# Performance work log

Measured on AMD Instinct MI355X. Metric: run time of the kernel, lower is better.

The kernel has to match this reference:

```python
import jax, jax.numpy as jnp
import numpy as np

B, L, D = 1, 4096, 1024
H = 16
HD = D // H
SCALE = HD ** -0.5


def setup_inputs() -> dict:
    key = jax.random.key(0)
    k1, k2, k3 = jax.random.split(key, 3)
    X = jax.random.normal(k1, (B, L, D), dtype=jnp.float32)
    # torch Linear default init ~ U(-1/sqrt(fan_in), 1/sqrt(fan_in)); scaled normals are fine for a reference
    Wqkv = jax.random.normal(k2, (D, 3 * D), dtype=jnp.float32) * (D ** -0.5)
    bqkv = jnp.zeros((3 * D,), dtype=jnp.float32)
    Wproj = jax.random.normal(k3, (D, D), dtype=jnp.float32) * (D ** -0.5)
    bproj = jnp.zeros((D,), dtype=jnp.float32)
    return {"X": X, "Wqkv": Wqkv, "bqkv": bqkv, "Wproj": Wproj, "bproj": bproj}


def reference(X, Wqkv, bqkv, Wproj, bproj):
    Bn, Ln, Dn = X.shape
    qkv = X @ Wqkv + bqkv                       # [B, L, 3D]
    qkv = qkv.reshape(Bn, Ln, 3, H, HD)
    q, k, v = qkv[:, :, 0], qkv[:, :, 1], qkv[:, :, 2]   # [B, L, H, HD]
    # attention scores [B, H, L, L] (naive, matches original)
    attn = jnp.einsum('bqhd,bkhd->bhqk', q, k) * SCALE
    causal = jnp.tril(jnp.ones((Ln, Ln), dtype=bool))     # True = keep
    attn = jnp.where(causal, attn, -jnp.inf)
    score = jax.nn.softmax(attn, axis=-1)
    out = jnp.einsum('bhqk,bkhd->bqhd', score, v)         # [B, L, H, HD]
    out = out.reshape(Bn, Ln, Dn)
    return out @ Wproj + bproj
```

## Files before the change

kernel.cpp:

```cpp
#include <hip/hip_runtime.h>
#include <hip/hip_bf16.h>


typedef unsigned short ushort_t;
typedef __attribute__((ext_vector_type(8))) short short8;
typedef __attribute__((ext_vector_type(4))) float f32x4;

#define MFMA16(a, b, c) __builtin_amdgcn_mfma_f32_16x16x32_bf16(a, b, c, 0, 0, 0)

static constexpr int Lq = 4096;
static constexpr int Dm = 1024;
static constexpr int NH = 16;
static constexpr int HD = 64;
static constexpr int D3 = 3072;
static constexpr float SCALE_LOG2E = 0.125f * 1.44269504088896340736f;

__device__ __forceinline__ ushort_t f2bf(float f) {
    union { float f; unsigned int u; } x{f};
    unsigned int u = x.u;
    u += 0x7fffu + ((u >> 16) & 1u);
    return (ushort_t)(u >> 16);
}

__device__ __forceinline__ void gl2lds16(const ushort_t* g, ushort_t* l) {
    __builtin_amdgcn_global_load_lds(
        (const __attribute__((address_space(1))) unsigned int*)g,
        (__attribute__((address_space(3))) unsigned int*)l, 16, 0, 0);
}

__global__ void cvt_bf16(const float* __restrict__ in, ushort_t* __restrict__ out, int n) {
    int i = (blockIdx.x * blockDim.x + threadIdx.x) * 4;
    if (i + 3 < n) {
        float4 v = *(const float4*)&in[i];
        ushort_t r[4] = { f2bf(v.x), f2bf(v.y), f2bf(v.z), f2bf(v.w) };
        *(uint2*)&out[i] = *(uint2*)r;
    }
}

__global__ void wtrans(const float* __restrict__ W, ushort_t* __restrict__ Wt, int K, int N) {
    __shared__ float tile[32][33];
    int nb = blockIdx.x * 32, kb = blockIdx.y * 32;
    int tx = threadIdx.x, ty = threadIdx.y;
    for (int j = 0; j < 32; j += 8)
        tile[ty + j][tx] = W[(size_t)(kb + ty + j) * N + nb + tx];
    __syncthreads();
    for (int j = 0; j < 32; j += 8)
        Wt[(size_t)(nb + ty + j) * K + kb + tx] = f2bf(tile[tx][ty + j]);
}

__global__ void vtrans(const ushort_t* __restrict__ qkv, ushort_t* __restrict__ Vt) {
    __shared__ ushort_t tile[32][33];
    int h  = blockIdx.z;
    int lb = blockIdx.x * 32;
    int db = blockIdx.y * 32;
    int tx = threadIdx.x, ty = threadIdx.y;
    for (int j = 0; j < 32; j += 8)
        tile[ty + j][tx] = qkv[(size_t)(lb + ty + j) * D3 + 2048 + h * HD + db + tx];
    __syncthreads();
    for (int j = 0; j < 32; j += 8)
        Vt[(size_t)h * HD * Lq + (size_t)(db + ty + j) * Lq + lb + tx] = tile[tx][ty + j];
}

template <bool OUT_BF16, bool QSCALE>
__global__ void __launch_bounds__(256)
gemm_bt(const ushort_t* __restrict__ A, const ushort_t* __restrict__ Bt,
        const float* __restrict__ bias, void* __restrict__ C,
        int M, int N, int K) {
    __shared__ alignas(16) ushort_t Alds[128 * 32];
    __shared__ alignas(16) ushort_t Blds[128 * 32];
    const int tid  = threadIdx.x;
    const int lane = tid & 63;
    const int w    = tid >> 6;
    const int quad = lane >> 4;
    const int l16  = lane & 15;
    const int mbase = blockIdx.x * 128;
    const int nbase = blockIdx.y * 128;
    const int moff  = (w >> 1) * 64;
    const int noff  = (w & 1) * 64;

    f32x4 acc[4][4] = {};

    for (int kb = 0; kb < K; kb += 32) {
        __syncthreads();
        #pragma unroll
        for (int c = 0; c < 2; c++) {
            int id  = w * 128 + c * 64 + lane;
            int row = id >> 2, col = (id & 3) * 8;
            gl2lds16(&A[(size_t)(mbase + row) * K + kb + col], &Alds[(size_t)(w * 128 + c * 64) * 8]);
            gl2lds16(&Bt[(size_t)(nbase + row) * K + kb + col], &Blds[(size_t)(w * 128 + c * 64) * 8]);
        }
        __syncthreads();
        short8 a[4], b[4];
        #pragma unroll
        for (int m = 0; m < 4; m++)
            a[m] = *(const short8*)&Alds[(moff + m * 16 + l16) * 32 + quad * 8];
        #pragma unroll
        for (int n = 0; n < 4; n++)
            b[n] = *(const short8*)&Blds[(noff + n * 16 + l16) * 32 + quad * 8];
        #pragma unroll
        for (int m = 0; m < 4; m++)
            #pragma unroll
            for (int n = 0; n < 4; n++)
                acc[m][n] = MFMA16(a[m], b[n], acc[m][n]);
    }

    #pragma unroll
    for (int m = 0; m < 4; m++)
        #pragma unroll
        for (int n = 0; n < 4; n++)
            #pragma unroll
            for (int r = 0; r < 4; r++) {
                int row = mbase + moff + m * 16 + quad * 4 + r;
                int col = nbase + noff + n * 16 + l16;
                float v = acc[m][n][r] + bias[col];
                if (QSCALE && col < Dm) v *= SCALE_LOG2E;
                if (OUT_BF16)
                    ((ushort_t*)C)[(size_t)row * N + col] = f2bf(v);
                else
                    ((float*)C)[(size_t)row * N + col] = v;
            }
}

__global__ void __launch_bounds__(256, 1)
attn_fwd(const ushort_t* __restrict__ qkv, const ushort_t* __restrict__ Vt,
         ushort_t* __restrict__ O) {
    __shared__ alignas(16) ushort_t Kl[2][64 * 64];
    __shared__ alignas(16) ushort_t Vl[2][64 * 64];
    __shared__ alignas(16) ushort_t Pl[4 * 32 * 72];

    const int tid  = threadIdx.x;
    const int lane = tid & 63;
    const int w    = tid >> 6;
    const int quad = lane >> 4;
    const int l16  = lane & 15;
    const int bid  = blockIdx.x;
    const int h    = bid & 15;
    const int p    = bid >> 4;
    ushort_t* pw   = Pl + w * 32 * 72;
    const float NEG_INF = -__builtin_inff();
    const int sw = l16 & 7;

    const short bf1 = (short)0x3F80;
    const short8 ones = { bf1, bf1, bf1, bf1, bf1, bf1, bf1, bf1 };

    const ushort_t* kbase = qkv + Dm + h * HD;
    const ushort_t* vbase = Vt + (size_t)h * HD * Lq;

    const int g0 = w * 128 + lane;
    const int r0 = g0 >> 3, c0 = (g0 & 7) ^ (r0 & 7);
    const int g1 = g0 + 64;
    const int r1 = g1 >> 3, c1 = (g1 & 7) ^ (r1 & 7);
    const ushort_t* ks0 = kbase + (size_t)r0 * D3 + c0 * 8;
    const ushort_t* ks1 = kbase + (size_t)r1 * D3 + c1 * 8;
    const ushort_t* vs0 = vbase + (size_t)r0 * Lq + c0 * 8;
    const ushort_t* vs1 = vbase + (size_t)r1 * Lq + c1 * 8;
    ushort_t* kd0[2] = { &Kl[0][w * 1024], &Kl[1][w * 1024] };
    ushort_t* kd1[2] = { &Kl[0][w * 1024 + 512], &Kl[1][w * 1024 + 512] };
    ushort_t* vd0[2] = { &Vl[0][w * 1024], &Vl[1][w * 1024] };
    ushort_t* vd1[2] = { &Vl[0][w * 1024 + 512], &Vl[1][w * 1024 + 512] };

    for (int sel = 0; sel < 2; sel++) {
        const int c  = sel ? (31 - p) : p;
        const int qc = c * 128;
        const int nt = 2 * c + 2;
        const int qw = qc + w * 32;

        short8 qf[2][2];
        #pragma unroll
        for (int m = 0; m < 2; m++) {
            const ushort_t* qr = qkv + (size_t)(qw + m * 16 + l16) * D3 + h * HD;
            qf[m][0] = *(const short8*)(qr + quad * 8);
            qf[m][1] = *(const short8*)(qr + 32 + quad * 8);
        }

        f32x4 o[2][4] = {};
        f32x4 lacc[2] = {};

        gl2lds16(ks0, kd0[0]);
        gl2lds16(ks1, kd1[0]);
        gl2lds16(vs0, vd0[0]);
        gl2lds16(vs1, vd1[0]);

        for (int kt = 0; kt < nt; kt++) {
            const int buf = kt & 1;
            __syncthreads();
            if (kt + 1 < nt) {
                const size_t ko = (size_t)(kt + 1) * 64 * D3;
                const int    vo = (kt + 1) * 64;
                gl2lds16(ks0 + ko, kd0[buf ^ 1]);
                gl2lds16(ks1 + ko, kd1[buf ^ 1]);
                gl2lds16(vs0 + vo, vd0[buf ^ 1]);
                gl2lds16(vs1 + vo, vd1[buf ^ 1]);
            }
            const int k0 = kt * 64;

            short8 kf[4][2];
            #pragma unroll
            for (int s = 0; s < 4; s++)
                #pragma unroll
                for (int kh = 0; kh < 2; kh++)
                    kf[s][kh] = *(const short8*)&Kl[buf][(s * 16 + l16) * 64 + (((kh * 4 + quad) ^ sw) * 8)];

            f32x4 st[2][4];
            #pragma unroll
            for (int m = 0; m < 2; m++)
                #pragma unroll
                for (int s = 0; s < 4; s++) {
                    f32x4 t = {};
                    t = MFMA16(qf[m][0], kf[s][0], t);
                    t = MFMA16(qf[m][1], kf[s][1], t);
                    st[m][s] = t;
                }

            #pragma unroll
            for (int m = 0; m < 2; m++)
                #pragma unroll
                for (int r = 0; r < 4; r++) {
                    const int qg = qw + m * 16 + quad * 4 + r;
                    ushort_t* prow = pw + (m * 16 + quad * 4 + r) * 72;
                    #pragma unroll
                    for (int s = 0; s < 4; s++) {
                        const int ki = k0 + s * 16 + l16;
                        float v = (ki > qg) ? NEG_INF : st[m][s][r];
                        prow[s * 16 + l16] = f2bf(__builtin_amdgcn_exp2f(v));
                    }
                }

            short8 pf[2][2];
            #pragma unroll
            for (int m = 0; m < 2; m++)
                #pragma unroll
                for (int kh = 0; kh < 2; kh++)
                    pf[m][kh] = *(const short8*)&pw[(m * 16 + l16) * 72 + kh * 32 + quad * 8];
            #pragma unroll
            for (int m = 0; m < 2; m++) {
                lacc[m] = MFMA16(pf[m][0], ones, lacc[m]);
                lacc[m] = MFMA16(pf[m][1], ones, lacc[m]);
            }

            short8 vf[4][2];
            #pragma unroll
            for (int t = 0; t < 4; t++)
                #pragma unroll
                for (int kh = 0; kh < 2; kh++)
                    vf[t][kh] = *(const short8*)&Vl[buf][(t * 16 + l16) * 64 + (((kh * 4 + quad) ^ sw) * 8)];
            #pragma unroll
            for (int m = 0; m < 2; m++)
                #pragma unroll
                for (int t = 0; t < 4; t++) {
                    o[m][t] = MFMA16(pf[m][0], vf[t][0], o[m][t]);
                    o[m][t] = MFMA16(pf[m][1], vf[t][1], o[m][t]);
                }
        }

        #pragma unroll
        for (int m = 0; m < 2; m++)
            #pragma unroll
            for (int r = 0; r < 4; r++) {
                const float inv = 1.0f / lacc[m][r];
                ushort_t* orow = O + (size_t)(qw + m * 16 + quad * 4 + r) * Dm + h * HD;
                #pragma unroll
                for (int t = 0; t < 4; t++)
                    orow[t * 16 + l16] = f2bf(o[m][t][r] * inv);
            }
        __syncthreads();
    }
}

extern "C" void kernel_launch(void* const* d_in, const int* in_sizes, int n_in,
                              void* d_out, int out_size, void* d_ws, size_t ws_size,
                              hipStream_t stream) {
    const float* X     = (const float*)d_in[0];
    const float* Wqkv  = (const float*)d_in[1];
    const float* bqkv  = (const float*)d_in[2];
    const float* Wproj = (const float*)d_in[3];
    const float* bproj = (const float*)d_in[4];
    float* out = (float*)d_out;

    ushort_t* ws     = (ushort_t*)d_ws;
    ushort_t* Xb     = ws;
    ushort_t* WqkvT  = Xb + (size_t)Lq * Dm;
    ushort_t* WprojT = WqkvT + (size_t)D3 * Dm;
    ushort_t* qkvB   = WprojT + (size_t)Dm * Dm;
    ushort_t* VtB    = qkvB + (size_t)Lq * D3;
    ushort_t* Ob     = VtB + (size_t)NH * HD * Lq;

    cvt_bf16<<<(Lq * Dm / 4 + 255) / 256, 256, 0, stream>>>(X, Xb, Lq * Dm);
    wtrans<<<dim3(D3 / 32, Dm / 32), dim3(32, 8), 0, stream>>>(Wqkv, WqkvT, Dm, D3);
    wtrans<<<dim3(Dm / 32, Dm / 32), dim3(32, 8), 0, stream>>>(Wproj, WprojT, Dm, Dm);

    gemm_bt<true, true><<<dim3(Lq / 128, D3 / 128), 256, 0, stream>>>(
        Xb, WqkvT, bqkv, (void*)qkvB, Lq, D3, Dm);

    vtrans<<<dim3(Lq / 32, HD / 32, NH), dim3(32, 8), 0, stream>>>(qkvB, VtB);

    attn_fwd<<<dim3(256), 256, 0, stream>>>(qkvB, VtB, Ob);

    gemm_bt<false, false><<<dim3(Lq / 128, Dm / 128), 256, 0, stream>>>(
        Ob, WprojT, bproj, (void*)out, Lq, Dm, Dm);
}
```

Measured before the change: 237.7 us.

## Use 8 waves per attention block and permute V keys for packed P stores

The attention kernel now runs 512 threads, eight waves of 16 query rows each, instead of four waves of 32 rows. Each thread issues one K and one V async load per tile instead of two of each. The V transpose permutes key order within each 64-key tile so every lane writes four exponentials as a single packed 8-byte LDS store rather than four scalar stores. This adds latency hiding and cuts LDS store instructions, but each wave now reads the full K/V tiles for half as many rows, which doubles LDS read traffic per unit of work.

```diff
diff --git a/kernel.cpp b/kernel.cpp
--- a/kernel.cpp
+++ b/kernel.cpp
@@ -20,6 +20,13 @@
     unsigned int u = x.u;
     u += 0x7fffu + ((u >> 16) & 1u);
     return (ushort_t)(u >> 16);
+}
+
+__device__ __forceinline__ unsigned int pack2bf(float a, float b) {
+    union { float f; unsigned int u; } xa{a}, xb{b};
+    unsigned int ua = xa.u + (0x7fffu + ((xa.u >> 16) & 1u));
+    unsigned int ub = xb.u + (0x7fffu + ((xb.u >> 16) & 1u));
+    return (ua >> 16) | (ub & 0xffff0000u);
 }
 
 __device__ __forceinline__ void gl2lds16(const ushort_t* g, ushort_t* l) {
@@ -57,8 +64,11 @@
     for (int j = 0; j < 32; j += 8)
         tile[ty + j][tx] = qkv[(size_t)(lb + ty + j) * D3 + 2048 + h * HD + db + tx];
     __syncthreads();
-    for (int j = 0; j < 32; j += 8)
-        Vt[(size_t)h * HD * Lq + (size_t)(db + ty + j) * Lq + lb + tx] = tile[tx][ty + j];
+    const int key  = lb + tx;
+    const int k63  = key & 63;
+    const int cp   = (key & ~63) + ((k63 & 15) * 4 + (k63 >> 4));
+    for (int j = 0; j < 32; j += 8)
+        Vt[(size_t)h * HD * Lq + (size_t)(db + ty + j) * Lq + cp] = tile[tx][ty + j];
 }
 
 template <bool OUT_BF16, bool QSCALE>
@@ -121,12 +131,12 @@
             }
 }
 
-__global__ void __launch_bounds__(256, 1)
+__global__ void __launch_bounds__(512, 1)
 attn_fwd(const ushort_t* __restrict__ qkv, const ushort_t* __restrict__ Vt,
          ushort_t* __restrict__ O) {
     __shared__ alignas(16) ushort_t Kl[2][64 * 64];
     __shared__ alignas(16) ushort_t Vl[2][64 * 64];
-    __shared__ alignas(16) ushort_t Pl[4 * 32 * 72];
+    __shared__ alignas(16) ushort_t Pl[8 * 16 * 72];
 
     const int tid  = threadIdx.x;
     const int lane = tid & 63;
@@ -136,7 +146,7 @@
     const int bid  = blockIdx.x;
     const int h    = bid & 15;
     const int p    = bid >> 4;
-    ushort_t* pw   = Pl + w * 32 * 72;
+    ushort_t* pw   = Pl + w * 16 * 72;
     const float NEG_INF = -__builtin_inff();
     const int sw = l16 & 7;
 
@@ -146,51 +156,35 @@
     const ushort_t* kbase = qkv + Dm + h * HD;
     const ushort_t* vbase = Vt + (size_t)h * HD * Lq;
 
-    const int g0 = w * 128 + lane;
-    const int r0 = g0 >> 3, c0 = (g0 & 7) ^ (r0 & 7);
-    const int g1 = g0 + 64;
-    const int r1 = g1 >> 3, c1 = (g1 & 7) ^ (r1 & 7);
-    const ushort_t* ks0 = kbase + (size_t)r0 * D3 + c0 * 8;
-    const ushort_t* ks1 = kbase + (size_t)r1 * D3 + c1 * 8;
-    const ushort_t* vs0 = vbase + (size_t)r0 * Lq + c0 * 8;
-    const ushort_t* vs1 = vbase + (size_t)r1 * Lq + c1 * 8;
-    ushort_t* kd0[2] = { &Kl[0][w * 1024], &Kl[1][w * 1024] };
-    ushort_t* kd1[2] = { &Kl[0][w * 1024 + 512], &Kl[1][w * 1024 + 512] };
-    ushort_t* vd0[2] = { &Vl[0][w * 1024], &Vl[1][w * 1024] };
-    ushort_t* vd1[2] = { &Vl[0][w * 1024 + 512], &Vl[1][w * 1024 + 512] };
+    const int gr = tid;
+    const int rr = gr >> 3, cc = (gr & 7) ^ (rr & 7);
+    const ushort_t* ks = kbase + (size_t)rr * D3 + cc * 8;
+    const ushort_t* vs = vbase + (size_t)rr * Lq + cc * 8;
+    ushort_t* kd[2] = { &Kl[0][w * 512], &Kl[1][w * 512] };
+    ushort_t* vd[2] = { &Vl[0][w * 512], &Vl[1][w * 512] };
 
     for (int sel = 0; sel < 2; sel++) {
         const int c  = sel ? (31 - p) : p;
         const int qc = c * 128;
         const int nt = 2 * c + 2;
-        const int qw = qc + w * 32;
-
-        short8 qf[2][2];
-        #pragma unroll
-        for (int m = 0; m < 2; m++) {
-            const ushort_t* qr = qkv + (size_t)(qw + m * 16 + l16) * D3 + h * HD;
-            qf[m][0] = *(const short8*)(qr + quad * 8);
-            qf[m][1] = *(const short8*)(qr + 32 + quad * 8);
-        }
-
-        f32x4 o[2][4] = {};
-        f32x4 lacc[2] = {};
-
-        gl2lds16(ks0, kd0[0]);
-        gl2lds16(ks1, kd1[0]);
-        gl2lds16(vs0, vd0[0]);
-        gl2lds16(vs1, vd1[0]);
+        const int qw = qc + w * 16;
+
+        const ushort_t* qr = qkv + (size_t)(qw + l16) * D3 + h * HD;
+        const short8 qf0 = *(const short8*)(qr + quad * 8);
+        const short8 qf1 = *(const short8*)(qr + 32 + quad * 8);
+
+        f32x4 o[4] = {};
+        f32x4 lacc = {};
+
+        gl2lds16(ks, kd[0]);
+        gl2lds16(vs, vd[0]);
 
         for (int kt = 0; kt < nt; kt++) {
             const int buf = kt & 1;
             __syncthreads();
             if (kt + 1 < nt) {
-                const size_t ko = (size_t)(kt + 1) * 64 * D3;
-                const int    vo = (kt + 1) * 64;
-                gl2lds16(ks0 + ko, kd0[buf ^ 1]);
-                gl2lds16(ks1 + ko, kd1[buf ^ 1]);
-                gl2lds16(vs0 + vo, vd0[buf ^ 1]);
-                gl2lds16(vs1 + vo, vd1[buf ^ 1]);
+                gl2lds16(ks + (size_t)(kt + 1) * 64 * D3, kd[buf ^ 1]);
+                gl2lds16(vs + (kt + 1) * 64, vd[buf ^ 1]);
             }
             const int k0 = kt * 64;
 
@@ -201,68 +195,50 @@
                 for (int kh = 0; kh < 2; kh++)
                     kf[s][kh] = *(const short8*)&Kl[buf][(s * 16 + l16) * 64 + (((kh * 4 + quad) ^ sw) * 8)];
 
-            f32x4 st[2][4];
-            #pragma unroll
-            for (int m = 0; m < 2; m++)
+            f32x4 st[4];
+            #pragma unroll
+            for (int s = 0; s < 4; s++) {
+                f32x4 t = {};
+                t = MFMA16(qf0, kf[s][0], t);
+                t = MFMA16(qf1, kf[s][1], t);
+                st[s] = t;
+            }
+
+            #pragma unroll
+            for (int r = 0; r < 4; r++) {
+                const int qg = qw + quad * 4 + r;
+                float e[4];
                 #pragma unroll
                 for (int s = 0; s < 4; s++) {
-                    f32x4 t = {};
-                    t = MFMA16(qf[m][0], kf[s][0], t);
-                    t = MFMA16(qf[m][1], kf[s][1], t);
-                    st[m][s] = t;
+                    const int ki = k0 + s * 16 + l16;
+                    e[s] = __builtin_amdgcn_exp2f((ki > qg) ? NEG_INF : st[s][r]);
                 }
-
-            #pragma unroll
-            for (int m = 0; m < 2; m++)
-                #pragma unroll
-                for (int r = 0; r < 4; r++) {
-                    const int qg = qw + m * 16 + quad * 4 + r;
-                    ushort_t* prow = pw + (m * 16 + quad * 4 + r) * 72;
-                    #pragma unroll
-                    for (int s = 0; s < 4; s++) {
-                        const int ki = k0 + s * 16 + l16;
-                        float v = (ki > qg) ? NEG_INF : st[m][s][r];
-                        prow[s * 16 + l16] = f2bf(__builtin_amdgcn_exp2f(v));
-                    }
-                }
-
-            short8 pf[2][2];
-            #pragma unroll
-            for (int m = 0; m < 2; m++)
-                #pragma unroll
-                for (int kh = 0; kh < 2; kh++)
-                    pf[m][kh] = *(const short8*)&pw[(m * 16 + l16) * 72 + kh * 32 + quad * 8];
-            #pragma unroll
-            for (int m = 0; m < 2; m++) {
-                lacc[m] = MFMA16(pf[m][0], ones, lacc[m]);
-                lacc[m] = MFMA16(pf[m][1], ones, lacc[m]);
-            }
-
-            short8 vf[4][2];
+                uint2 pk = { pack2bf(e[0], e[1]), pack2bf(e[2], e[3]) };
+                *(uint2*)&pw[(quad * 4 + r) * 72 + l16 * 4] = pk;
+            }
+
+            const short8 pf0 = *(const short8*)&pw[l16 * 72 + quad * 8];
+            const short8 pf1 = *(const short8*)&pw[l16 * 72 + 32 + quad * 8];
+            lacc = MFMA16(pf0, ones, lacc);
+            lacc = MFMA16(pf1, ones, lacc);
+
+            #pragma unroll
+            for (int t = 0; t < 4; t++) {
+                short8 vf0 = *(const short8*)&Vl[buf][(t * 16 + l16) * 64 + ((quad ^ sw) * 8)];
+                short8 vf1 = *(const short8*)&Vl[buf][(t * 16 + l16) * 64 + (((4 + quad) ^ sw) * 8)];
+                o[t] = MFMA16(pf0, vf0, o[t]);
+                o[t] = MFMA16(pf1, vf1, o[t]);
+            }
+        }
+
+        #pragma unroll
+        for (int r = 0; r < 4; r++) {
+            const float inv = 1.0f / lacc[r];
+            ushort_t* orow = O + (size_t)(qw + quad * 4 + r) * Dm + h * HD;
             #pragma unroll
             for (int t = 0; t < 4; t++)
-                #pragma unroll
-                for (int kh = 0; kh < 2; kh++)
-                    vf[t][kh] = *(const short8*)&Vl[buf][(t * 16 + l16) * 64 + (((kh * 4 + quad) ^ sw) * 8)];
-            #pragma unroll
-            for (int m = 0; m < 2; m++)
-                #pragma unroll
-                for (int t = 0; t < 4; t++) {
-                    o[m][t] = MFMA16(pf[m][0], vf[t][0], o[m][t]);
-                    o[m][t] = MFMA16(pf[m][1], vf[t][1], o[m][t]);
-                }
+                orow[t * 16 + l16] = f2bf(o[t][r] * inv);
         }
-
-        #pragma unroll
-        for (int m = 0; m < 2; m++)
-            #pragma unroll
-            for (int r = 0; r < 4; r++) {
-                const float inv = 1.0f / lacc[m][r];
-                ushort_t* orow = O + (size_t)(qw + m * 16 + quad * 4 + r) * Dm + h * HD;
-                #pragma unroll
-                for (int t = 0; t < 4; t++)
-                    orow[t * 16 + l16] = f2bf(o[m][t][r] * inv);
-            }
         __syncthreads();
     }
 }
@@ -294,7 +270,7 @@
 
     vtrans<<<dim3(Lq / 32, HD / 32, NH), dim3(32, 8), 0, stream>>>(qkvB, VtB);
 
-    attn_fwd<<<dim3(256), 256, 0, stream>>>(qkvB, VtB, Ob);
+    attn_fwd<<<dim3(256), 512, 0, stream>>>(qkvB, VtB, Ob);
 
     gemm_bt<false, false><<<dim3(Lq / 128, Dm / 128), 256, 0, stream>>>(
         Ob, WprojT, bproj, (void*)out, Lq, Dm, Dm);
```

Result: faster. 224.3 us (-5.6%).

## Split attention into one q-chunk per block, peel masked tiles, pack P stores

Applied to the files above, without the earlier changes.

The attention kernel now launches one block per (head, 128-row query chunk), 512 blocks with a two-block occupancy hint, instead of pairing chunks p and 31-p inside one block. Blocks are ordered so the longest chunks start first. The key loop is unrolled by two with static double-buffer indices, and only the final two diagonal tiles apply the causal mask. V^T columns are permuted within each 64-key group so each lane writes its four P values as one packed bf16x2 store, using the hardware convert instead of a manual rounding routine. This trades the built-in load balancing of chunk pairing for more resident blocks and less per-element mask and store work.

```diff
diff --git a/kernel.cpp b/kernel.cpp
--- a/kernel.cpp
+++ b/kernel.cpp
@@ -1,5 +1,6 @@
 #include <hip/hip_runtime.h>
 #include <hip/hip_bf16.h>
+#include <string.h>
 
 
 typedef unsigned short ushort_t;
@@ -20,6 +21,13 @@
     unsigned int u = x.u;
     u += 0x7fffu + ((u >> 16) & 1u);
     return (ushort_t)(u >> 16);
+}
+
+__device__ __forceinline__ unsigned int cvtpk(float a, float b) {
+    __hip_bfloat162 h = __float22bfloat162_rn(make_float2(a, b));
+    unsigned int u;
+    memcpy(&u, &h, 4);
+    return u;
 }
 
 __device__ __forceinline__ void gl2lds16(const ushort_t* g, ushort_t* l) {
@@ -57,8 +65,11 @@
     for (int j = 0; j < 32; j += 8)
         tile[ty + j][tx] = qkv[(size_t)(lb + ty + j) * D3 + 2048 + h * HD + db + tx];
     __syncthreads();
+    const int key  = lb + tx;
+    const int k63  = key & 63;
+    const int cp   = (key & ~63) + ((k63 & 15) * 4 + (k63 >> 4));
     for (int j = 0; j < 32; j += 8)
-        Vt[(size_t)h * HD * Lq + (size_t)(db + ty + j) * Lq + lb + tx] = tile[tx][ty + j];
+        Vt[(size_t)h * HD * Lq + (size_t)(db + ty + j) * Lq + cp] = tile[tx][ty + j];
 }
 
 template <bool OUT_BF16, bool QSCALE>
@@ -121,7 +132,7 @@
             }
 }
 
-__global__ void __launch_bounds__(256, 1)
+__global__ void __launch_bounds__(256, 2)
 attn_fwd(const ushort_t* __restrict__ qkv, const ushort_t* __restrict__ Vt,
          ushort_t* __restrict__ O) {
     __shared__ alignas(16) ushort_t Kl[2][64 * 64];
@@ -135,16 +146,36 @@
     const int l16  = lane & 15;
     const int bid  = blockIdx.x;
     const int h    = bid & 15;
-    const int p    = bid >> 4;
+    const int c    = 31 - (bid >> 4);
+    const int qc   = c * 128;
+    const int qw   = qc + w * 32;
     ushort_t* pw   = Pl + w * 32 * 72;
     const float NEG_INF = -__builtin_inff();
-    const int sw = l16 & 7;
+    const int sw   = l16 & 7;
 
     const short bf1 = (short)0x3F80;
     const short8 ones = { bf1, bf1, bf1, bf1, bf1, bf1, bf1, bf1 };
 
     const ushort_t* kbase = qkv + Dm + h * HD;
     const ushort_t* vbase = Vt + (size_t)h * HD * Lq;
+
+    short8 qf[2][2];
+    #pragma unroll
+    for (int m = 0; m < 2; m++) {
+        const ushort_t* qr = qkv + (size_t)(qw + m * 16 + l16) * D3 + h * HD;
+        qf[m][0] = *(const short8*)(qr + quad * 8);
+        qf[m][1] = *(const short8*)(qr + 32 + quad * 8);
+    }
+
+    f32x4 o[2][4] = {};
+    f32x4 lacc[2] = {};
+
+    int kvo[4][2];
+    #pragma unroll
+    for (int s = 0; s < 4; s++)
+        #pragma unroll
+        for (int kh = 0; kh < 2; kh++)
+            kvo[s][kh] = (s * 16 + l16) * 64 + (((kh * 4 + quad) ^ sw) * 8);
 
     const int g0 = w * 128 + lane;
     const int r0 = g0 >> 3, c0 = (g0 & 7) ^ (r0 & 7);
@@ -154,117 +185,106 @@
     const ushort_t* ks1 = kbase + (size_t)r1 * D3 + c1 * 8;
     const ushort_t* vs0 = vbase + (size_t)r0 * Lq + c0 * 8;
     const ushort_t* vs1 = vbase + (size_t)r1 * Lq + c1 * 8;
-    ushort_t* kd0[2] = { &Kl[0][w * 1024], &Kl[1][w * 1024] };
-    ushort_t* kd1[2] = { &Kl[0][w * 1024 + 512], &Kl[1][w * 1024 + 512] };
-    ushort_t* vd0[2] = { &Vl[0][w * 1024], &Vl[1][w * 1024] };
-    ushort_t* vd1[2] = { &Vl[0][w * 1024 + 512], &Vl[1][w * 1024 + 512] };
-
-    for (int sel = 0; sel < 2; sel++) {
-        const int c  = sel ? (31 - p) : p;
-        const int qc = c * 128;
-        const int nt = 2 * c + 2;
-        const int qw = qc + w * 32;
-
-        short8 qf[2][2];
-        #pragma unroll
-        for (int m = 0; m < 2; m++) {
-            const ushort_t* qr = qkv + (size_t)(qw + m * 16 + l16) * D3 + h * HD;
-            qf[m][0] = *(const short8*)(qr + quad * 8);
-            qf[m][1] = *(const short8*)(qr + 32 + quad * 8);
-        }
-
-        f32x4 o[2][4] = {};
-        f32x4 lacc[2] = {};
-
-        gl2lds16(ks0, kd0[0]);
-        gl2lds16(ks1, kd1[0]);
-        gl2lds16(vs0, vd0[0]);
-        gl2lds16(vs1, vd1[0]);
-
-        for (int kt = 0; kt < nt; kt++) {
-            const int buf = kt & 1;
-            __syncthreads();
-            if (kt + 1 < nt) {
-                const size_t ko = (size_t)(kt + 1) * 64 * D3;
-                const int    vo = (kt + 1) * 64;
-                gl2lds16(ks0 + ko, kd0[buf ^ 1]);
-                gl2lds16(ks1 + ko, kd1[buf ^ 1]);
-                gl2lds16(vs0 + vo, vd0[buf ^ 1]);
-                gl2lds16(vs1 + vo, vd1[buf ^ 1]);
+
+    auto stage = [&](int t, int b) {
+        const size_t ko = (size_t)t * 64 * D3;
+        const int    vo = t * 64;
+        gl2lds16(ks0 + ko, &Kl[b][w * 1024]);
+        gl2lds16(ks1 + ko, &Kl[b][w * 1024 + 512]);
+        gl2lds16(vs0 + vo, &Vl[b][w * 1024]);
+        gl2lds16(vs1 + vo, &Vl[b][w * 1024 + 512]);
+    };
+
+    auto compute = [&](const ushort_t* Kb, const ushort_t* Vb, int k0, bool domask) {
+        short8 kf[4][2];
+        #pragma unroll
+        for (int s = 0; s < 4; s++)
+            #pragma unroll
+            for (int kh = 0; kh < 2; kh++)
+                kf[s][kh] = *(const short8*)&Kb[kvo[s][kh]];
+
+        f32x4 st[2][4];
+        #pragma unroll
+        for (int m = 0; m < 2; m++)
+            #pragma unroll
+            for (int s = 0; s < 4; s++) {
+                f32x4 t = {};
+                t = MFMA16(qf[m][0], kf[s][0], t);
+                t = MFMA16(qf[m][1], kf[s][1], t);
+                st[m][s] = t;
             }
-            const int k0 = kt * 64;
-
-            short8 kf[4][2];
-            #pragma unroll
-            for (int s = 0; s < 4; s++)
-                #pragma unroll
-                for (int kh = 0; kh < 2; kh++)
-                    kf[s][kh] = *(const short8*)&Kl[buf][(s * 16 + l16) * 64 + (((kh * 4 + quad) ^ sw) * 8)];
-
-            f32x4 st[2][4];
-            #pragma unroll
-            for (int m = 0; m < 2; m++)
+
+        #pragma unroll
+        for (int m = 0; m < 2; m++)
+            #pragma unroll
+            for (int r = 0; r < 4; r++) {
+                float e[4];
                 #pragma unroll
                 for (int s = 0; s < 4; s++) {
-                    f32x4 t = {};
-                    t = MFMA16(qf[m][0], kf[s][0], t);
-                    t = MFMA16(qf[m][1], kf[s][1], t);
-                    st[m][s] = t;
+                    float v = st[m][s][r];
+                    if (domask) {
+                        const int qg = qw + m * 16 + quad * 4 + r;
+                        if (k0 + s * 16 + l16 > qg) v = NEG_INF;
+                    }
+                    e[s] = __builtin_amdgcn_exp2f(v);
                 }
-
-            #pragma unroll
-            for (int m = 0; m < 2; m++)
-                #pragma unroll
-                for (int r = 0; r < 4; r++) {
-                    const int qg = qw + m * 16 + quad * 4 + r;
-                    ushort_t* prow = pw + (m * 16 + quad * 4 + r) * 72;
-                    #pragma unroll
-                    for (int s = 0; s < 4; s++) {
-                        const int ki = k0 + s * 16 + l16;
-                        float v = (ki > qg) ? NEG_INF : st[m][s][r];
-                        prow[s * 16 + l16] = f2bf(__builtin_amdgcn_exp2f(v));
-                    }
-                }
-
-            short8 pf[2][2];
-            #pragma unroll
-            for (int m = 0; m < 2; m++)
-                #pragma unroll
-                for (int kh = 0; kh < 2; kh++)
-                    pf[m][kh] = *(const short8*)&pw[(m * 16 + l16) * 72 + kh * 32 + quad * 8];
-            #pragma unroll
-            for (int m = 0; m < 2; m++) {
-                lacc[m] = MFMA16(pf[m][0], ones, lacc[m]);
-                lacc[m] = MFMA16(pf[m][1], ones, lacc[m]);
+                uint2 pk = { cvtpk(e[0], e[1]), cvtpk(e[2], e[3]) };
+                *(uint2*)&pw[(m * 16 + quad * 4 + r) * 72 + l16 * 4] = pk;
             }
 
-            short8 vf[4][2];
+        short8 pf[2][2];
+        #pragma unroll
+        for (int m = 0; m < 2; m++)
+            #pragma unroll
+            for (int kh = 0; kh < 2; kh++)
+                pf[m][kh] = *(const short8*)&pw[(m * 16 + l16) * 72 + kh * 32 + quad * 8];
+        #pragma unroll
+        for (int m = 0; m < 2; m++) {
+            lacc[m] = MFMA16(pf[m][0], ones, lacc[m]);
+            lacc[m] = MFMA16(pf[m][1], ones, lacc[m]);
+        }
+
+        short8 vf[4][2];
+        #pragma unroll
+        for (int t = 0; t < 4; t++)
+            #pragma unroll
+            for (int kh = 0; kh < 2; kh++)
+                vf[t][kh] = *(const short8*)&Vb[kvo[t][kh]];
+        #pragma unroll
+        for (int m = 0; m < 2; m++)
+            #pragma unroll
+            for (int t = 0; t < 4; t++) {
+                o[m][t] = MFMA16(pf[m][0], vf[t][0], o[m][t]);
+                o[m][t] = MFMA16(pf[m][1], vf[t][1], o[m][t]);
+            }
+    };
+
+    stage(0, 0);
+
+    for (int kt2 = 0; kt2 < c; kt2++) {
+        __syncthreads();
+        stage(2 * kt2 + 1, 1);
+        compute(Kl[0], Vl[0], (2 * kt2) * 64, false);
+        __syncthreads();
+        stage(2 * kt2 + 2, 0);
+        compute(Kl[1], Vl[1], (2 * kt2 + 1) * 64, false);
+    }
+    __syncthreads();
+    stage(2 * c + 1, 1);
+    compute(Kl[0], Vl[0], 2 * c * 64, true);
+    __syncthreads();
+    compute(Kl[1], Vl[1], 2 * c * 64 + 64, true);
+
+    #pragma unroll
+    for (int m = 0; m < 2; m++)
+        #pragma unroll
+        for (int r = 0; r < 4; r++) {
+            const float inv = 1.0f / lacc[m][r];
+            ushort_t* orow = O + (size_t)(qw + m * 16 + quad * 4 + r) * Dm + h * HD;
             #pragma unroll
             for (int t = 0; t < 4; t++)
-                #pragma unroll
-                for (int kh = 0; kh < 2; kh++)
-                    vf[t][kh] = *(const short8*)&Vl[buf][(t * 16 + l16) * 64 + (((kh * 4 + quad) ^ sw) * 8)];
-            #pragma unroll
-            for (int m = 0; m < 2; m++)
-                #pragma unroll
-                for (int t = 0; t < 4; t++) {
-                    o[m][t] = MFMA16(pf[m][0], vf[t][0], o[m][t]);
-                    o[m][t] = MFMA16(pf[m][1], vf[t][1], o[m][t]);
-                }
+                orow[t * 16 + l16] = f2bf(o[m][t][r] * inv);
         }
-
-        #pragma unroll
-        for (int m = 0; m < 2; m++)
-            #pragma unroll
-            for (int r = 0; r < 4; r++) {
-                const float inv = 1.0f / lacc[m][r];
-                ushort_t* orow = O + (size_t)(qw + m * 16 + quad * 4 + r) * Dm + h * HD;
-                #pragma unroll
-                for (int t = 0; t < 4; t++)
-                    orow[t * 16 + l16] = f2bf(o[m][t][r] * inv);
-            }
-        __syncthreads();
-    }
 }
 
 extern "C" void kernel_launch(void* const* d_in, const int* in_sizes, int n_in,
@@ -294,7 +314,7 @@
 
     vtrans<<<dim3(Lq / 32, HD / 32, NH), dim3(32, 8), 0, stream>>>(qkvB, VtB);
 
-    attn_fwd<<<dim3(256), 256, 0, stream>>>(qkvB, VtB, Ob);
+    attn_fwd<<<dim3(512), 256, 0, stream>>>(qkvB, VtB, Ob);
 
     gemm_bt<false, false><<<dim3(Lq / 128, Dm / 128), 256, 0, stream>>>(
         Ob, WprojT, bproj, (void*)out, Lq, Dm, Dm);
```

Measured after the change: 232.7 us. 2.1% less time.
